# Kernel tuning notes

Hardware: AMD Instinct MI355X
Metric: run time of the kernel (lower is better)

Reference implementation:

```python
import jax, jax.numpy as jnp
import numpy as np

B = 32768    # number of trees (batch)
N = 10       # nodes per tree (forced by Linear(embed_dim*10, ...))
L = 10       # leaf tokens per subtree (also 10, same cat constraint)
E = 16       # embed_dim
H = 8        # hidden_dim
V = 2000     # embed_dict_size
LAT = 128    # latent_vector_dim
EPS = 1e-5   # BatchNorm1d eps


def setup_inputs() -> dict:
    key = jax.random.key(0)
    ks = jax.random.split(key, 17)
    w = lambda k, shape, s=0.05: (jax.random.normal(k, shape, jnp.float32) * s)
    return {
        "tokens": jax.random.randint(ks[0], (B, N, L), 0, V),
        "emb":    w(ks[1], (V, E), 0.1),            # nn.Embedding weight
        "w_ih":   w(ks[2], (4 * E, E)),             # LSTM input weights (i,f,g,o)
        "b_ih":   w(ks[3], (4 * E,)),
        "b_hh":   w(ks[4], (4 * E,)),               # h0=c0=0 so W_hh never contributes
        "ffW1":   w(ks[5], (4 * E, 10 * E)),        # child_sum_ff Linear(160,64)
        "ffb1":   w(ks[6], (4 * E,)),
        "ffW2":   w(ks[7], (E, 4 * E)),             # child_sum_ff Linear(64,16)
        "ffb2":   w(ks[8], (E,)),
        "fmW":    w(ks[9], (H, E)),                 # ff_model Linear(16,8)
        "fmb":    w(ks[10], (H,)),
        "tsW":    w(ks[11], (1, H)),                # tail_score Linear(8,1)
        "tsb":    w(ks[12], (1,)),
        "suW":    w(ks[13], (LAT, H)),              # tail_summary Linear(8,latent)
        "sub_b":  w(ks[14], (LAT,)),
        "gamma":  jnp.ones((LAT,), jnp.float32),    # BatchNorm1d affine
        "beta":   jnp.zeros((LAT,), jnp.float32),
    }


def _child_ff(x, W1, b1, W2, b2):
    # nn.Sequential(Linear(160,64), ReLU, Linear(64,16))
    return jax.nn.relu(x @ W1.T + b1) @ W2.T + b2


def _lstm_single_step(x, w_ih, b_ih, b_hh):
    # One-timestep LSTM with zero initial (h, c); PyTorch gate order i,f,g,o.
    gates = x @ w_ih.T + b_ih + b_hh
    i, f, g, o = jnp.split(gates, 4, axis=-1)
    c = jax.nn.sigmoid(i) * jnp.tanh(g)          # f * c0 = 0
    return jax.nn.sigmoid(o) * jnp.tanh(c)


def reference(tokens, emb, w_ih, b_ih, b_hh, ffW1, ffb1, ffW2, ffb2,
              fmW, fmb, tsW, tsb, suW, sub_b, gamma, beta):
    leaf = emb[tokens]                                        # (B,N,L,E) gather
    subtree = _child_ff(leaf.reshape(B, N, L * E),
                        ffW1, ffb1, ffW2, ffb2)               # (B,N,E)
    h = _lstm_single_step(subtree, w_ih, b_ih, b_hh)          # (B,N,E)
    code = _child_ff(h.reshape(B, N * E), ffW1, ffb1, ffW2, ffb2)  # (B,E)
    ff_out = code @ fmW.T + fmb                               # (B,H)
    score = jnp.tanh(ff_out @ tsW.T + tsb)                    # (B,1)
    s = ff_out @ suW.T + sub_b                                # (B,LAT)
    mu = jnp.mean(s, axis=0)
    var = jnp.var(s, axis=0)                                  # biased, training-mode BN
    summary = gamma * (s - mu) / jnp.sqrt(var + EPS) + beta
    return score, summary
```

## Files before the change

kernel.cpp:

```cpp
#include <hip/hip_runtime.h>
#include <hip/hip_bf16.h>

#define BB 32768
#define NN 10
#define VV 2000
#define EPSBN 1e-5

__global__ __launch_bounds__(256) void k_table(const float* __restrict__ emb,
                                               const float* __restrict__ W1,
                                               float* __restrict__ T1) {
  int idx = blockIdx.x * 256 + threadIdx.x;
  if (idx >= VV * 640) return;
  int v = idx / 640;
  int r = idx - v * 640;
  int l = r >> 6;
  int o = r & 63;
  const float* e = emb + v * 16;
  const float* w = W1 + o * 160 + l * 16;
  float s = 0.f;
#pragma unroll
  for (int k = 0; k < 16; ++k) s = fmaf(e[k], w[k], s);
  T1[idx] = s;
}

__global__ __launch_bounds__(256) void k_fuse(const float* __restrict__ w_ih,
    const float* __restrict__ b_ih, const float* __restrict__ b_hh,
    const float* __restrict__ W2, const float* __restrict__ b2v,
    float* __restrict__ W3T, float* __restrict__ bias3T) {
  int idx = blockIdx.x * 256 + threadIdx.x;
  if (idx < 3072) {
    int k = idx / 48, jj = idx - k * 48;
    int gr = (jj < 16) ? jj : jj + 16;
    float s = 0.f;
#pragma unroll
    for (int o = 0; o < 16; ++o) s = fmaf(w_ih[gr * 16 + o], W2[o * 64 + k], s);
    W3T[idx] = s;
  } else if (idx < 3120) {
    int jj = idx - 3072;
    int gr = (jj < 16) ? jj : jj + 16;
    float s = b_ih[gr] + b_hh[gr];
#pragma unroll
    for (int o = 0; o < 16; ++o) s = fmaf(w_ih[gr * 16 + o], b2v[o], s);
    bias3T[jj] = s;
  }
}

__global__ __launch_bounds__(256, 3) void k_stage1(const int* __restrict__ tokens,
    const float* __restrict__ T1, const float* __restrict__ b1v,
    const float* __restrict__ W3T_and_bias,
    float* __restrict__ hbuf) {
  __shared__ __align__(16) float w_lds[3120];
  const int tid = threadIdx.x;
  for (int i = tid; i < 780; i += 256)
    ((float4*)w_lds)[i] = ((const float4*)W3T_and_bias)[i];

  const int item = blockIdx.x * 256 + tid;
  int tk[10];
  {
    const int2* tp2 = (const int2*)(tokens + (size_t)item * 10);
#pragma unroll
    for (int q = 0; q < 5; ++q) { int2 t = tp2[q]; tk[2 * q] = t.x; tk[2 * q + 1] = t.y; }
  }
  __syncthreads();

  float4 h[16];
  {
    const float4* r = (const float4*)(T1 + (size_t)tk[0] * 640);
#pragma unroll
    for (int c = 0; c < 16; ++c) h[c] = r[c];
  }
#pragma unroll
  for (int l = 1; l < 10; ++l) {
    const float4* r = (const float4*)(T1 + (size_t)tk[l] * 640 + l * 64);
#pragma unroll
    for (int c = 0; c < 16; ++c) {
      float4 v = r[c];
      h[c].x += v.x; h[c].y += v.y; h[c].z += v.z; h[c].w += v.w;
    }
  }
  float h1[64];
  {
    const float4* b1q = (const float4*)b1v;
#pragma unroll
    for (int c = 0; c < 16; ++c) {
      float4 bq = b1q[c];
      h1[4 * c]     = fmaxf(h[c].x + bq.x, 0.f);
      h1[4 * c + 1] = fmaxf(h[c].y + bq.y, 0.f);
      h1[4 * c + 2] = fmaxf(h[c].z + bq.z, 0.f);
      h1[4 * c + 3] = fmaxf(h[c].w + bq.w, 0.f);
    }
  }

  float acc[48];
#pragma unroll
  for (int j4 = 0; j4 < 12; ++j4) {
    float4 b = *(const float4*)&w_lds[3072 + j4 * 4];
    acc[4 * j4] = b.x; acc[4 * j4 + 1] = b.y; acc[4 * j4 + 2] = b.z; acc[4 * j4 + 3] = b.w;
  }
#pragma unroll
  for (int k = 0; k < 64; ++k) {
    const float hk = h1[k];
#pragma unroll
    for (int j4 = 0; j4 < 12; ++j4) {
      float4 w = *(const float4*)&w_lds[k * 48 + j4 * 4];
      acc[4 * j4]     = fmaf(w.x, hk, acc[4 * j4]);
      acc[4 * j4 + 1] = fmaf(w.y, hk, acc[4 * j4 + 1]);
      acc[4 * j4 + 2] = fmaf(w.z, hk, acc[4 * j4 + 2]);
      acc[4 * j4 + 3] = fmaf(w.w, hk, acc[4 * j4 + 3]);
    }
  }

  float res[16];
#pragma unroll
  for (int j = 0; j < 16; ++j) {
    float si = __builtin_amdgcn_rcpf(1.f + __expf(-acc[j]));
    float tg = fmaf(2.f, __builtin_amdgcn_rcpf(1.f + __expf(-2.f * acc[16 + j])), -1.f);
    float so = __builtin_amdgcn_rcpf(1.f + __expf(-acc[32 + j]));
    float c = si * tg;
    float th = fmaf(2.f, __builtin_amdgcn_rcpf(1.f + __expf(-2.f * c)), -1.f);
    res[j] = so * th;
  }
  float4* op = (float4*)(hbuf + (size_t)item * 16);
#pragma unroll
  for (int q = 0; q < 4; ++q)
    op[q] = make_float4(res[4 * q], res[4 * q + 1], res[4 * q + 2], res[4 * q + 3]);
}

__global__ __launch_bounds__(256) void k_stage2(const float* __restrict__ hbuf,
    const float* __restrict__ W1, const float* __restrict__ b1v,
    const float* __restrict__ W2, const float* __restrict__ b2v,
    const float* __restrict__ fmW, const float* __restrict__ fmb,
    const float* __restrict__ tsW, const float* __restrict__ tsb,
    const float* __restrict__ suW, const float* __restrict__ sub_b,
    float* __restrict__ out, float* __restrict__ partials) {
  __shared__ float h1b_lds[32 * 68];
  __shared__ float code_lds[32 * 20];
  __shared__ float ff_lds[32 * 12];
  int tid = threadIdx.x;
  int lane = tid & 63;
  int wid = __builtin_amdgcn_readfirstlane(tid >> 6);
  int treeBase = blockIdx.x * 32;
  {
    int tw = treeBase + wid * 8;
    float acc[8];
#pragma unroll
    for (int t = 0; t < 8; ++t) acc[t] = b1v[lane];
    const float* wrow = W1 + lane * 160;
    const float* xbase = hbuf + (size_t)tw * 160;
    for (int k = 0; k < 160; k += 4) {
      float4 wv = *(const float4*)(wrow + k);
#pragma unroll
      for (int t = 0; t < 8; ++t) {
        float4 xv = *(const float4*)(xbase + t * 160 + k);
        acc[t] = fmaf(wv.x, xv.x, acc[t]);
        acc[t] = fmaf(wv.y, xv.y, acc[t]);
        acc[t] = fmaf(wv.z, xv.z, acc[t]);
        acc[t] = fmaf(wv.w, xv.w, acc[t]);
      }
    }
#pragma unroll
    for (int t = 0; t < 8; ++t)
      h1b_lds[(wid * 8 + t) * 68 + lane] = fmaxf(acc[t], 0.f);
  }
  __syncthreads();
  {
    int t2 = tid >> 3, jj = tid & 7;
    float c0 = b2v[jj], c1 = b2v[jj + 8];
    const float* w2a = W2 + jj * 64;
    const float* w2b = W2 + (jj + 8) * 64;
    const float* hb = &h1b_lds[t2 * 68];
    for (int o = 0; o < 64; o += 4) {
      float4 hv = *(const float4*)(hb + o);
      float4 a4 = *(const float4*)(w2a + o);
      float4 b4 = *(const float4*)(w2b + o);
      c0 = fmaf(a4.x, hv.x, c0); c0 = fmaf(a4.y, hv.y, c0);
      c0 = fmaf(a4.z, hv.z, c0); c0 = fmaf(a4.w, hv.w, c0);
      c1 = fmaf(b4.x, hv.x, c1); c1 = fmaf(b4.y, hv.y, c1);
      c1 = fmaf(b4.z, hv.z, c1); c1 = fmaf(b4.w, hv.w, c1);
    }
    code_lds[t2 * 20 + jj] = c0;
    code_lds[t2 * 20 + jj + 8] = c1;
  }
  __syncthreads();
  {
    int t = tid >> 3, q = tid & 7;
    float f = fmb[q];
    const float* cw = fmW + q * 16;
    const float* cl = &code_lds[t * 20];
#pragma unroll
    for (int j4 = 0; j4 < 16; j4 += 4) {
      float4 cv = *(const float4*)(cl + j4);
      float4 wv = *(const float4*)(cw + j4);
      f = fmaf(wv.x, cv.x, f); f = fmaf(wv.y, cv.y, f);
      f = fmaf(wv.z, cv.z, f); f = fmaf(wv.w, cv.w, f);
    }
    ff_lds[t * 12 + q] = f;
  }
  __syncthreads();
  {
    int t = tid >> 3, r = tid & 7;
    float4 f0 = *(const float4*)&ff_lds[t * 12];
    float4 f1 = *(const float4*)&ff_lds[t * 12 + 4];
    int tree = treeBase + t;
    float* od = out + (size_t)BB + (size_t)tree * 128 + r * 16;
#pragma unroll
    for (int cc = 0; cc < 16; ++cc) {
      int c = r * 16 + cc;
      const float* u = suW + c * 8;
      float4 u0 = *(const float4*)(u);
      float4 u1 = *(const float4*)(u + 4);
      float sv = sub_b[c];
      sv = fmaf(u0.x, f0.x, sv); sv = fmaf(u0.y, f0.y, sv);
      sv = fmaf(u0.z, f0.z, sv); sv = fmaf(u0.w, f0.w, sv);
      sv = fmaf(u1.x, f1.x, sv); sv = fmaf(u1.y, f1.y, sv);
      sv = fmaf(u1.z, f1.z, sv); sv = fmaf(u1.w, f1.w, sv);
      od[cc] = sv;
    }
    if (tid < 32) {
      int tt = tid;
      float4 g0 = *(const float4*)&ff_lds[tt * 12];
      float4 g1 = *(const float4*)&ff_lds[tt * 12 + 4];
      float sc = tsb[0];
      sc = fmaf(tsW[0], g0.x, sc); sc = fmaf(tsW[1], g0.y, sc);
      sc = fmaf(tsW[2], g0.z, sc); sc = fmaf(tsW[3], g0.w, sc);
      sc = fmaf(tsW[4], g1.x, sc); sc = fmaf(tsW[5], g1.y, sc);
      sc = fmaf(tsW[6], g1.z, sc); sc = fmaf(tsW[7], g1.w, sc);
      out[treeBase + tt] = tanhf(sc);
    }
  }
  {
    int waveId = blockIdx.x * 4 + wid;
    float* pw = partials + (size_t)waveId * 88;
#pragma unroll
    for (int rep = 0; rep < 2; ++rep) {
      int e = lane + rep * 64;
      if (e < 81) {
        int i = e / 9, jx = e - i * 9;
        float m = 0.f;
#pragma unroll
        for (int t = 0; t < 8; ++t) {
          const float* fr = &ff_lds[(wid * 8 + t) * 12];
          float fi = (i  < 8) ? fr[i]  : 1.f;
          float fj = (jx < 8) ? fr[jx] : 1.f;
          m = fmaf(fi, fj, m);
        }
        pw[e] = m;
      }
    }
  }
}

__global__ __launch_bounds__(256) void k_reduce(const float* __restrict__ partials,
                                                double* __restrict__ Msum) {
  __shared__ double red[256];
  int e = blockIdx.x;
  double s = 0.0;
  for (int w = threadIdx.x; w < 4096; w += 256)
    s += (double)partials[(size_t)w * 88 + e];
  red[threadIdx.x] = s;
  __syncthreads();
  for (int off = 128; off > 0; off >>= 1) {
    if (threadIdx.x < off) red[threadIdx.x] += red[threadIdx.x + off];
    __syncthreads();
  }
  if (threadIdx.x == 0) Msum[e] = red[0];
}

__global__ __launch_bounds__(128) void k_stats(const double* __restrict__ Msum,
    const float* __restrict__ suW, const float* __restrict__ sub_b,
    const float* __restrict__ gamma, const float* __restrict__ beta,
    float* __restrict__ statsA, float* __restrict__ statsB) {
  int c = threadIdx.x;
  double u[9];
#pragma unroll
  for (int q = 0; q < 8; ++q) u[q] = (double)suW[c * 8 + q];
  u[8] = (double)sub_b[c];
  double S1 = 0.0;
#pragma unroll
  for (int i = 0; i < 9; ++i) S1 += u[i] * Msum[72 + i];
  double mu = S1 / (double)BB;
  double E2 = 0.0;
#pragma unroll
  for (int i = 0; i < 9; ++i) {
    double acc = 0.0;
#pragma unroll
    for (int jx = 0; jx < 9; ++jx) acc += u[jx] * Msum[i * 9 + jx];
    E2 += u[i] * acc;
  }
  E2 /= (double)BB;
  double var = E2 - mu * mu;
  if (var < 0.0) var = 0.0;
  double rs = 1.0 / sqrt(var + (double)EPSBN);
  double A = (double)gamma[c] * rs;
  statsA[c] = (float)A;
  statsB[c] = (float)((double)beta[c] - mu * A);
}

__global__ __launch_bounds__(256) void k_norm(float* __restrict__ out,
    const float* __restrict__ statsA, const float* __restrict__ statsB) {
  int idx = blockIdx.x * 256 + threadIdx.x;
  float4* p = (float4*)(out + BB);
  float4 v = p[idx];
  int c4 = idx & 31;
  float4 a = ((const float4*)statsA)[c4];
  float4 b = ((const float4*)statsB)[c4];
  v.x = fmaf(v.x, a.x, b.x);
  v.y = fmaf(v.y, a.y, b.y);
  v.z = fmaf(v.z, a.z, b.z);
  v.w = fmaf(v.w, a.w, b.w);
  p[idx] = v;
}

extern "C" void kernel_launch(void* const* d_in, const int* in_sizes, int n_in,
                              void* d_out, int out_size, void* d_ws, size_t ws_size,
                              hipStream_t stream) {
  const int*   tokens = (const int*)d_in[0];
  const float* emb   = (const float*)d_in[1];
  const float* w_ih  = (const float*)d_in[2];
  const float* b_ih  = (const float*)d_in[3];
  const float* b_hh  = (const float*)d_in[4];
  const float* ffW1  = (const float*)d_in[5];
  const float* ffb1  = (const float*)d_in[6];
  const float* ffW2  = (const float*)d_in[7];
  const float* ffb2  = (const float*)d_in[8];
  const float* fmW   = (const float*)d_in[9];
  const float* fmb   = (const float*)d_in[10];
  const float* tsW   = (const float*)d_in[11];
  const float* tsb   = (const float*)d_in[12];
  const float* suW   = (const float*)d_in[13];
  const float* sub_b = (const float*)d_in[14];
  const float* gamma = (const float*)d_in[15];
  const float* beta  = (const float*)d_in[16];
  float* out = (float*)d_out;
  float* ws = (float*)d_ws;

  float*  T1       = ws;
  float*  hbuf     = T1 + 1280000;
  float*  partials = hbuf + 5242880;
  double* Msum     = (double*)(partials + 360448);
  float*  statsA   = (float*)(Msum + 82);
  float*  statsB   = statsA + 128;
  float*  W3T      = statsB + 128;
  float*  bias3T   = W3T + 3072;

  hipLaunchKernelGGL(k_table,  dim3(5000), dim3(256), 0, stream, emb, ffW1, T1);
  hipLaunchKernelGGL(k_fuse,   dim3(13),   dim3(256), 0, stream,
                     w_ih, b_ih, b_hh, ffW2, ffb2, W3T, bias3T);
  hipLaunchKernelGGL(k_stage1, dim3(1280), dim3(256), 0, stream,
                     tokens, T1, ffb1, W3T, hbuf);
  hipLaunchKernelGGL(k_stage2, dim3(1024), dim3(256), 0, stream,
                     hbuf, ffW1, ffb1, ffW2, ffb2, fmW, fmb, tsW, tsb, suW, sub_b,
                     out, partials);
  hipLaunchKernelGGL(k_reduce, dim3(81),   dim3(256), 0, stream, partials, Msum);
  hipLaunchKernelGGL(k_stats,  dim3(1),    dim3(128), 0, stream,
                     Msum, suW, sub_b, gamma, beta, statsA, statsB);
  hipLaunchKernelGGL(k_norm,   dim3(4096), dim3(256), 0, stream, out, statsA, statsB);
}
```

Baseline: 216.8 us.

## Unfuse W2·W_ih product in stage1, fold b1 into table, drop fuse kernel

Result: slower. 245.9 us (+13.4%).

```diff
diff --git a/kernel.cpp b/kernel.cpp
--- a/kernel.cpp
+++ b/kernel.cpp
@@ -6,63 +6,35 @@
 #define VV 2000
 #define EPSBN 1e-5
 
-__global__ __launch_bounds__(256) void k_table(const float* __restrict__ emb,
-                                               const float* __restrict__ W1,
-                                               float* __restrict__ T1) {
+__global__ __launch_bounds__(256) void k_prep(const float* __restrict__ emb,
+    const float* __restrict__ W1, const float* __restrict__ b1v,
+    float* __restrict__ T1) {
   int idx = blockIdx.x * 256 + threadIdx.x;
-  if (idx >= VV * 640) return;
   int v = idx / 640;
   int r = idx - v * 640;
   int l = r >> 6;
   int o = r & 63;
   const float* e = emb + v * 16;
   const float* w = W1 + o * 160 + l * 16;
-  float s = 0.f;
+  float s = (l == 0) ? b1v[o] : 0.f;
 #pragma unroll
   for (int k = 0; k < 16; ++k) s = fmaf(e[k], w[k], s);
   T1[idx] = s;
 }
 
-__global__ __launch_bounds__(256) void k_fuse(const float* __restrict__ w_ih,
+__global__ __attribute__((amdgpu_waves_per_eu(4, 5)))
+__launch_bounds__(256) void k_lstm(const int* __restrict__ tokens,
+    const float* __restrict__ T1, const float* __restrict__ W2,
+    const float* __restrict__ b2v, const float* __restrict__ w_ih,
     const float* __restrict__ b_ih, const float* __restrict__ b_hh,
-    const float* __restrict__ W2, const float* __restrict__ b2v,
-    float* __restrict__ W3T, float* __restrict__ bias3T) {
-  int idx = blockIdx.x * 256 + threadIdx.x;
-  if (idx < 3072) {
-    int k = idx / 48, jj = idx - k * 48;
-    int gr = (jj < 16) ? jj : jj + 16;
-    float s = 0.f;
-#pragma unroll
-    for (int o = 0; o < 16; ++o) s = fmaf(w_ih[gr * 16 + o], W2[o * 64 + k], s);
-    W3T[idx] = s;
-  } else if (idx < 3120) {
-    int jj = idx - 3072;
-    int gr = (jj < 16) ? jj : jj + 16;
-    float s = b_ih[gr] + b_hh[gr];
-#pragma unroll
-    for (int o = 0; o < 16; ++o) s = fmaf(w_ih[gr * 16 + o], b2v[o], s);
-    bias3T[jj] = s;
-  }
-}
-
-__global__ __launch_bounds__(256, 3) void k_stage1(const int* __restrict__ tokens,
-    const float* __restrict__ T1, const float* __restrict__ b1v,
-    const float* __restrict__ W3T_and_bias,
     float* __restrict__ hbuf) {
-  __shared__ __align__(16) float w_lds[3120];
-  const int tid = threadIdx.x;
-  for (int i = tid; i < 780; i += 256)
-    ((float4*)w_lds)[i] = ((const float4*)W3T_and_bias)[i];
-
-  const int item = blockIdx.x * 256 + tid;
+  const int item = blockIdx.x * 256 + threadIdx.x;
   int tk[10];
   {
-    const int2* tp2 = (const int2*)(tokens + (size_t)item * 10);
-#pragma unroll
-    for (int q = 0; q < 5; ++q) { int2 t = tp2[q]; tk[2 * q] = t.x; tk[2 * q + 1] = t.y; }
-  }
-  __syncthreads();
-
+    const int2* p = (const int2*)(tokens + (size_t)item * 10);
+#pragma unroll
+    for (int q = 0; q < 5; ++q) { int2 t = p[q]; tk[2 * q] = t.x; tk[2 * q + 1] = t.y; }
+  }
   float4 h[16];
   {
     const float4* r = (const float4*)(T1 + (size_t)tk[0] * 640);
@@ -78,52 +50,67 @@
       h[c].x += v.x; h[c].y += v.y; h[c].z += v.z; h[c].w += v.w;
     }
   }
-  float h1[64];
-  {
-    const float4* b1q = (const float4*)b1v;
-#pragma unroll
-    for (int c = 0; c < 16; ++c) {
-      float4 bq = b1q[c];
-      h1[4 * c]     = fmaxf(h[c].x + bq.x, 0.f);
-      h1[4 * c + 1] = fmaxf(h[c].y + bq.y, 0.f);
-      h1[4 * c + 2] = fmaxf(h[c].z + bq.z, 0.f);
-      h1[4 * c + 3] = fmaxf(h[c].w + bq.w, 0.f);
-    }
-  }
-
-  float acc[48];
-#pragma unroll
-  for (int j4 = 0; j4 < 12; ++j4) {
-    float4 b = *(const float4*)&w_lds[3072 + j4 * 4];
-    acc[4 * j4] = b.x; acc[4 * j4 + 1] = b.y; acc[4 * j4 + 2] = b.z; acc[4 * j4 + 3] = b.w;
-  }
-#pragma unroll
-  for (int k = 0; k < 64; ++k) {
-    const float hk = h1[k];
-#pragma unroll
-    for (int j4 = 0; j4 < 12; ++j4) {
-      float4 w = *(const float4*)&w_lds[k * 48 + j4 * 4];
-      acc[4 * j4]     = fmaf(w.x, hk, acc[4 * j4]);
-      acc[4 * j4 + 1] = fmaf(w.y, hk, acc[4 * j4 + 1]);
-      acc[4 * j4 + 2] = fmaf(w.z, hk, acc[4 * j4 + 2]);
-      acc[4 * j4 + 3] = fmaf(w.w, hk, acc[4 * j4 + 3]);
-    }
-  }
-
-  float res[16];
-#pragma unroll
-  for (int j = 0; j < 16; ++j) {
-    float si = __builtin_amdgcn_rcpf(1.f + __expf(-acc[j]));
-    float tg = fmaf(2.f, __builtin_amdgcn_rcpf(1.f + __expf(-2.f * acc[16 + j])), -1.f);
-    float so = __builtin_amdgcn_rcpf(1.f + __expf(-acc[32 + j]));
-    float c = si * tg;
-    float th = fmaf(2.f, __builtin_amdgcn_rcpf(1.f + __expf(-2.f * c)), -1.f);
-    res[j] = so * th;
-  }
+#pragma unroll
+  for (int c = 0; c < 16; ++c) {
+    h[c].x = fmaxf(h[c].x, 0.f); h[c].y = fmaxf(h[c].y, 0.f);
+    h[c].z = fmaxf(h[c].z, 0.f); h[c].w = fmaxf(h[c].w, 0.f);
+  }
+
+  float code[16];
+#pragma unroll
+  for (int c = 0; c < 16; ++c) {
+    const float4* wr = (const float4*)(W2 + c * 64);
+    float a = b2v[c];
+#pragma unroll
+    for (int k = 0; k < 16; ++k) {
+      float4 w = wr[k];
+      a = fmaf(w.x, h[k].x, a); a = fmaf(w.y, h[k].y, a);
+      a = fmaf(w.z, h[k].z, a); a = fmaf(w.w, h[k].w, a);
+    }
+    code[c] = a;
+  }
+
+  float act[3][16];
+#pragma unroll
+  for (int s = 0; s < 3; ++s) {
+    const int gr0 = (s == 0) ? 0 : (s == 1) ? 32 : 48;
+#pragma unroll
+    for (int j = 0; j < 16; ++j) {
+      const int gr = gr0 + j;
+      const float4* wr = (const float4*)(w_ih + gr * 16);
+      float a = b_ih[gr] + b_hh[gr];
+#pragma unroll
+      for (int c4 = 0; c4 < 4; ++c4) {
+        float4 w = wr[c4];
+        a = fmaf(w.x, code[4 * c4], a);
+        a = fmaf(w.y, code[4 * c4 + 1], a);
+        a = fmaf(w.z, code[4 * c4 + 2], a);
+        a = fmaf(w.w, code[4 * c4 + 3], a);
+      }
+      if (s == 1) {
+        float e = __expf(-2.f * a);
+        act[s][j] = fmaf(2.f, __builtin_amdgcn_rcpf(1.f + e), -1.f);
+      } else {
+        float e = __expf(-a);
+        act[s][j] = __builtin_amdgcn_rcpf(1.f + e);
+      }
+    }
+  }
+
   float4* op = (float4*)(hbuf + (size_t)item * 16);
 #pragma unroll
-  for (int q = 0; q < 4; ++q)
-    op[q] = make_float4(res[4 * q], res[4 * q + 1], res[4 * q + 2], res[4 * q + 3]);
+  for (int q = 0; q < 4; ++q) {
+    float r4[4];
+#pragma unroll
+    for (int u = 0; u < 4; ++u) {
+      int j = 4 * q + u;
+      float cc = act[0][j] * act[1][j];
+      float e2 = __expf(-2.f * cc);
+      float th = fmaf(2.f, __builtin_amdgcn_rcpf(1.f + e2), -1.f);
+      r4[u] = act[2][j] * th;
+    }
+    op[q] = make_float4(r4[0], r4[1], r4[2], r4[3]);
+  }
 }
 
 __global__ __launch_bounds__(256) void k_stage2(const float* __restrict__ hbuf,
@@ -340,14 +327,10 @@
   double* Msum     = (double*)(partials + 360448);
   float*  statsA   = (float*)(Msum + 82);
   float*  statsB   = statsA + 128;
-  float*  W3T      = statsB + 128;
-  float*  bias3T   = W3T + 3072;
-
-  hipLaunchKernelGGL(k_table,  dim3(5000), dim3(256), 0, stream, emb, ffW1, T1);
-  hipLaunchKernelGGL(k_fuse,   dim3(13),   dim3(256), 0, stream,
-                     w_ih, b_ih, b_hh, ffW2, ffb2, W3T, bias3T);
-  hipLaunchKernelGGL(k_stage1, dim3(1280), dim3(256), 0, stream,
-                     tokens, T1, ffb1, W3T, hbuf);
+
+  hipLaunchKernelGGL(k_prep,   dim3(5000), dim3(256), 0, stream, emb, ffW1, ffb1, T1);
+  hipLaunchKernelGGL(k_lstm,   dim3(1280), dim3(256), 0, stream,
+                     tokens, T1, ffW2, ffb2, w_ih, b_ih, b_hh, hbuf);
   hipLaunchKernelGGL(k_stage2, dim3(1024), dim3(256), 0, stream,
                      hbuf, ffW1, ffb1, ffW2, ffb2, fmW, fmb, tsW, tsb, suW, sub_b,
                      out, partials);
```
